# Kernel tuning notes

Hardware: AMD Instinct MI355X
Metric: run time of the kernel (lower is better)

## Reference

```python
import jax, jax.numpy as jnp
import numpy as np

T, B = 80, 256                 # timesteps (max objs per image), num sequences (images)
OBJ_DIM, EMBED, HID = 4096, 200, 512
NCLS = 151                      # 150 VG classes + background
D = HID + OBJ_DIM + EMBED + 128 # decoder inputs_dim = 4936


def _packed_gather_idx():
    # descending lengths 80..41, mimicking a sorted PackedSequence
    lengths = np.array([T - (i * 40) // B for i in range(B)])
    idx = []
    for t in range(T):
        bs = int((lengths > t).sum())
        idx.extend(t * B + b for b in range(bs))
    return np.asarray(idx, dtype=np.int32)  # [15504]


def setup_inputs() -> dict:
    key = jax.random.key(0)
    ks = jax.random.split(key, 6)
    s = jnp.float32(0.02)
    return {
        "sequence": jax.random.normal(ks[0], (T, B, D), jnp.float32),
        "embed": jax.random.normal(ks[1], (NCLS + 1, EMBED), jnp.float32) * s,
        "W_in": jax.random.normal(ks[2], (6 * HID, D + EMBED), jnp.float32) * s,
        "b_in": jnp.zeros((6 * HID,), jnp.float32),
        "W_state": jax.random.normal(ks[3], (5 * HID, HID), jnp.float32) * s,
        "b_state": jnp.zeros((5 * HID,), jnp.float32),
        "W_out": jax.random.normal(ks[4], (NCLS, HID), jnp.float32) * s,
        "b_out": jnp.zeros((NCLS,), jnp.float32),
        "gather_idx": jnp.asarray(_packed_gather_idx()),
    }


def reference(sequence, embed, W_in, b_in, W_state, b_state, W_out, b_out, gather_idx):
    H = HID

    def step(carry, x_t):
        h, c, prev_embed = carry
        ti = jnp.concatenate([x_t, prev_embed], axis=1)          # [B, D+E]
        pi = ti @ W_in.T + b_in                                   # [B, 6H]
        ps = h @ W_state.T + b_state                              # [B, 5H]
        i_g = jax.nn.sigmoid(pi[:, 0*H:1*H] + ps[:, 0*H:1*H])
        f_g = jax.nn.sigmoid(pi[:, 1*H:2*H] + ps[:, 1*H:2*H])
        m_i = jnp.tanh(pi[:, 2*H:3*H] + ps[:, 2*H:3*H])
        o_g = jax.nn.sigmoid(pi[:, 3*H:4*H] + ps[:, 3*H:4*H])
        c_new = i_g * m_i + f_g * c
        out = o_g * jnp.tanh(c_new)
        hw_g = jax.nn.sigmoid(pi[:, 4*H:5*H] + ps[:, 4*H:5*H])
        h_new = hw_g * out + (1.0 - hw_g) * pi[:, 5*H:6*H]        # highway
        pred = h_new @ W_out.T + b_out                            # [B, NCLS]
        # softmax is monotonic: argmax of softmax(pred)[:,1:] == argmax of pred[:,1:]
        best = jnp.argmax(pred[:, 1:], axis=1) + 1                # [B], in [1, NCLS-1]
        pe_new = embed[best + 1]                                  # [B, E]
        return (h_new, c_new, pe_new), (pred, best)

    h0 = jnp.zeros((B, HID), sequence.dtype)
    c0 = jnp.zeros((B, HID), sequence.dtype)
    pe0 = jnp.broadcast_to(embed[0], (B, EMBED))                  # 'start' token embed
    _, (dists, commits) = jax.lax.scan(step, (h0, c0, pe0), sequence)
    # packed (timestep-major) flattening of valid entries only
    out_dists = dists.reshape(T * B, NCLS)[gather_idx]            # [N, NCLS]
    out_commits = commits.reshape(T * B)[gather_idx]              # [N]
    return out_dists, out_commits
```

## Files before the change

### kernel.cpp

```cpp
#include <hip/hip_runtime.h>
#include <cstddef>
#include <cstdint>

#define T_STEPS 80
#define BATCH   256
#define DIM     4936
#define EMB     200
#define DE      5136
#define HID     512
#define SIXH    3072
#define FIVEH   2560
#define NCLS    151
#define NPACK   15504
#define NKT     156
#define NKT_H   16
#define NCOMB   2816

typedef unsigned short ushort_t;
typedef short short8 __attribute__((ext_vector_type(8)));
typedef float f32x4 __attribute__((ext_vector_type(4)));

__device__ inline ushort_t f2bf_rn(float x) {
    union { float f; uint32_t u; } v; v.f = x;
    uint32_t u = v.u;
    return (ushort_t)((u + 0x7FFFu + ((u >> 16) & 1u)) >> 16);
}
__device__ inline float bf2f(ushort_t b) {
    union { float f; uint32_t u; } v; v.u = ((uint32_t)b) << 16;
    return v.f;
}
__device__ inline float sigmoidf(float x) { return 1.f / (1.f + expf(-x)); }

__global__ __launch_bounds__(256) void convert_split(
    const float* __restrict__ src, int ld, int kvalid,
    ushort_t* __restrict__ hi, ushort_t* __restrict__ lo, int nktiles)
{
    __shared__ float s[128][33];
    const int tid = threadIdx.x;
    const int kt  = blockIdx.x;
    const int mt  = blockIdx.y;

#pragma unroll
    for (int it = 0; it < 4; ++it) {
        int idx = it * 256 + tid;
        int row = idx >> 3;
        int f4  = idx & 7;
        int k   = kt * 32 + f4 * 4;
        const float* p = src + (size_t)(mt * 128 + row) * ld + k;
        float4 v;
        if (k + 3 < kvalid) v = *(const float4*)p;
        else {
            v.x = (k + 0) < kvalid ? p[0] : 0.f;
            v.y = (k + 1) < kvalid ? p[1] : 0.f;
            v.z = (k + 2) < kvalid ? p[2] : 0.f;
            v.w = (k + 3) < kvalid ? p[3] : 0.f;
        }
        s[row][f4 * 4 + 0] = v.x; s[row][f4 * 4 + 1] = v.y;
        s[row][f4 * 4 + 2] = v.z; s[row][f4 * 4 + 3] = v.w;
    }
    __syncthreads();

    const size_t base = ((size_t)mt * nktiles + kt) * 4096;
#pragma unroll
    for (int it = 0; it < 2; ++it) {
        int o   = it * 256 + tid;
        int kb  = o >> 7;
        int row = o & 127;
        alignas(16) ushort_t hbuf[8];
        alignas(16) ushort_t lbuf[8];
#pragma unroll
        for (int e = 0; e < 8; ++e) {
            float x = s[row][kb * 8 + e];
            ushort_t hh = f2bf_rn(x);
            float lof = x - bf2f(hh);
            hbuf[e] = hh;
            lbuf[e] = f2bf_rn(lof);
        }
        *(uint4*)(hi + base + (size_t)o * 8) = *(const uint4*)hbuf;
        *(uint4*)(lo + base + (size_t)o * 8) = *(const uint4*)lbuf;
    }
}

__device__ inline void gload16(const ushort_t* g, ushort_t* l) {
    __builtin_amdgcn_global_load_lds(
        (const __attribute__((address_space(1))) void*)g,
        (__attribute__((address_space(3))) void*)l, 16, 0, 0);
}

__global__ __launch_bounds__(256) void mfma3(
    const ushort_t* __restrict__ Ah, const ushort_t* __restrict__ Al,
    const ushort_t* __restrict__ Bh, const ushort_t* __restrict__ Bl,
    const float* __restrict__ bias, float* __restrict__ OUT,
    int nkt, int ldout)
{
    __shared__ ushort_t sAh[2][4096], sAl[2][4096], sBh[2][4096], sBl[2][4096];

    const int tid  = threadIdx.x;
    const int wave = tid >> 6;
    const int lane = tid & 63;
    const int mt = blockIdx.y, ntb = blockIdx.x;
    const int wr = wave >> 1, wc = wave & 1;

    f32x4 acc[4][4];
#pragma unroll
    for (int i = 0; i < 4; ++i)
#pragma unroll
        for (int j = 0; j < 4; ++j) acc[i][j] = (f32x4){0.f, 0.f, 0.f, 0.f};

    const size_t abase = (size_t)mt * nkt * 4096;
    const size_t bbase = (size_t)ntb * nkt * 4096;
    const int lw = wave * 512;
    const int kb = lane >> 4;
    const int lr = lane & 15;
    const int aoff = kb * 1024 + (wr * 64 + lr) * 8;
    const int boff = kb * 1024 + (wc * 64 + lr) * 8;

#define STAGE_PX(buf, kt_) do {                                     \
        const size_t ko = (size_t)(kt_) * 4096 + tid * 8;           \
        gload16(Ah + abase + ko,        &sAh[buf][lw]);             \
        gload16(Ah + abase + ko + 2048, &sAh[buf][2048 + lw]);      \
        gload16(Al + abase + ko,        &sAl[buf][lw]);             \
        gload16(Al + abase + ko + 2048, &sAl[buf][2048 + lw]);      \
        gload16(Bh + bbase + ko,        &sBh[buf][lw]);             \
        gload16(Bh + bbase + ko + 2048, &sBh[buf][2048 + lw]);      \
        gload16(Bl + bbase + ko,        &sBl[buf][lw]);             \
        gload16(Bl + bbase + ko + 2048, &sBl[buf][2048 + lw]);      \
    } while (0)

    STAGE_PX(0, 0);
    asm volatile("s_waitcnt vmcnt(0)" ::: "memory");
    __builtin_amdgcn_s_barrier();

    int cur = 0;
    for (int kt = 0; kt < nkt; ++kt) {
        if (kt + 1 < nkt) STAGE_PX(cur ^ 1, kt + 1);

        const ushort_t* pAh = sAh[cur];
        const ushort_t* pAl = sAl[cur];
        const ushort_t* pBh = sBh[cur];
        const ushort_t* pBl = sBl[cur];
        short8 ah[4], al[4], bh[4], bl[4];
#pragma unroll
        for (int i = 0; i < 4; ++i) {
            ah[i] = *(const short8*)&pAh[aoff + i * 128];
            al[i] = *(const short8*)&pAl[aoff + i * 128];
        }
#pragma unroll
        for (int j = 0; j < 4; ++j) {
            bh[j] = *(const short8*)&pBh[boff + j * 128];
            bl[j] = *(const short8*)&pBl[boff + j * 128];
        }
#pragma unroll
        for (int i = 0; i < 4; ++i)
#pragma unroll
            for (int j = 0; j < 4; ++j) {
                acc[i][j] = __builtin_amdgcn_mfma_f32_16x16x32_bf16(ah[i], bh[j], acc[i][j], 0, 0, 0);
                acc[i][j] = __builtin_amdgcn_mfma_f32_16x16x32_bf16(ah[i], bl[j], acc[i][j], 0, 0, 0);
                acc[i][j] = __builtin_amdgcn_mfma_f32_16x16x32_bf16(al[i], bh[j], acc[i][j], 0, 0, 0);
            }

        __builtin_amdgcn_sched_barrier(0);
        asm volatile("s_waitcnt vmcnt(0)" ::: "memory");
        __builtin_amdgcn_s_barrier();
        cur ^= 1;
    }
#undef STAGE_PX

#pragma unroll
    for (int i = 0; i < 4; ++i) {
        const int row = mt * 128 + wr * 64 + i * 16 + (lane >> 4) * 4;
#pragma unroll
        for (int j = 0; j < 4; ++j) {
            const int col = ntb * 128 + wc * 64 + j * 16 + (lane & 15);
            const float bv = bias[col];
#pragma unroll
            for (int r = 0; r < 4; ++r)
                OUT[(size_t)(row + r) * ldout + col] = acc[i][j][r] + bv;
        }
    }
}

__global__ __launch_bounds__(256) void ps_splitk(
    const ushort_t* __restrict__ hH, const ushort_t* __restrict__ hL,
    const ushort_t* __restrict__ WcH, const ushort_t* __restrict__ WcL,
    float* __restrict__ partial)
{
    __shared__ ushort_t sAh[8192], sAl[8192], sBh[8192], sBl[8192];

    const int tid  = threadIdx.x;
    const int wave = tid >> 6;
    const int lane = tid & 63;
    const int ntile = blockIdx.x;
    const int mtile = blockIdx.y;
    const int ks    = blockIdx.z;
    const int amt = mtile >> 1, arh = mtile & 1;
    const int bmt = ntile >> 1, brh = ntile & 1;
    const int wr = wave >> 1, wc = wave & 1;

    f32x4 acc[2][2];
#pragma unroll
    for (int i = 0; i < 2; ++i)
#pragma unroll
        for (int j = 0; j < 2; ++j) acc[i][j] = (f32x4){0.f, 0.f, 0.f, 0.f};

    const int lw    = wave * 512;
    const int lsrcA = wave * 1024 + arh * 512 + lane * 8;
    const int lsrcB = wave * 1024 + brh * 512 + lane * 8;

#pragma unroll
    for (int ki = 0; ki < 4; ++ki) {
        const int kt = ks * 4 + ki;
        const size_t atile = ((size_t)(amt * NKT_H + kt)) * 4096;
        const size_t btile = ((size_t)(bmt * NKT_H + kt)) * 4096;
        gload16(hH  + atile + lsrcA, &sAh[ki * 2048 + lw]);
        gload16(hL  + atile + lsrcA, &sAl[ki * 2048 + lw]);
        gload16(WcH + btile + lsrcB, &sBh[ki * 2048 + lw]);
        gload16(WcL + btile + lsrcB, &sBl[ki * 2048 + lw]);
    }
    __syncthreads();

    const int kb = lane >> 4;
    const int lr = lane & 15;
#pragma unroll
    for (int ki = 0; ki < 4; ++ki) {
        short8 ah[2], al[2], bh[2], bl[2];
#pragma unroll
        for (int i = 0; i < 2; ++i) {
            const int ao = ki * 2048 + kb * 512 + (wr * 32 + i * 16 + lr) * 8;
            ah[i] = *(const short8*)&sAh[ao];
            al[i] = *(const short8*)&sAl[ao];
        }
#pragma unroll
        for (int j = 0; j < 2; ++j) {
            const int bo = ki * 2048 + kb * 512 + (wc * 32 + j * 16 + lr) * 8;
            bh[j] = *(const short8*)&sBh[bo];
            bl[j] = *(const short8*)&sBl[bo];
        }
#pragma unroll
        for (int i = 0; i < 2; ++i)
#pragma unroll
            for (int j = 0; j < 2; ++j) {
                acc[i][j] = __builtin_amdgcn_mfma_f32_16x16x32_bf16(ah[i], bh[j], acc[i][j], 0, 0, 0);
                acc[i][j] = __builtin_amdgcn_mfma_f32_16x16x32_bf16(ah[i], bl[j], acc[i][j], 0, 0, 0);
                acc[i][j] = __builtin_amdgcn_mfma_f32_16x16x32_bf16(al[i], bh[j], acc[i][j], 0, 0, 0);
            }
    }

    float* out = partial + ((size_t)ks * 256 + mtile * 64) * NCOMB + ntile * 64;
#pragma unroll
    for (int i = 0; i < 2; ++i) {
        const int row = wr * 32 + i * 16 + (lane >> 4) * 4;
#pragma unroll
        for (int j = 0; j < 2; ++j) {
            const int col = wc * 32 + j * 16 + (lane & 15);
#pragma unroll
            for (int r = 0; r < 4; ++r)
                out[(size_t)(row + r) * NCOMB + col] = acc[i][j][r];
        }
    }
}

__global__ __launch_bounds__(256) void ew_gemm(
    const float* __restrict__ embed, const float* __restrict__ Win,
    float* __restrict__ EW)
{
    __shared__ float As[16][68];
    __shared__ float Bs[16][68];
    const int tid = threadIdx.x;
    const int tx  = tid & 15;
    const int ty  = tid >> 4;
    const int n0  = blockIdx.x * 64;
    const int m0  = blockIdx.y * 64;
    const int lrow = tid >> 2;
    const int lk   = (tid & 3) * 4;

    float acc[4][4];
#pragma unroll
    for (int i = 0; i < 4; ++i)
#pragma unroll
        for (int j = 0; j < 4; ++j) acc[i][j] = 0.f;

    for (int k0 = 0; k0 < EMB; k0 += 16) {
        int k = k0 + lk;
        float4 av = {0.f,0.f,0.f,0.f}, bv = {0.f,0.f,0.f,0.f};
        if (k < EMB) {
            int am = m0 + lrow;
            if (am < 152) av = *(const float4*)(embed + (size_t)am * EMB + k);
            bv = *(const float4*)(Win + (size_t)(n0 + lrow) * DE + DIM + k);
        }
        __syncthreads();
        As[lk + 0][lrow] = av.x; As[lk + 1][lrow] = av.y;
        As[lk + 2][lrow] = av.z; As[lk + 3][lrow] = av.w;
        Bs[lk + 0][lrow] = bv.x; Bs[lk + 1][lrow] = bv.y;
        Bs[lk + 2][lrow] = bv.z; Bs[lk + 3][lrow] = bv.w;
        __syncthreads();
#pragma unroll
        for (int kk = 0; kk < 16; ++kk) {
            float4 a4 = *(const float4*)&As[kk][ty * 4];
            float4 b4 = *(const float4*)&Bs[kk][tx * 4];
            float avr[4] = {a4.x, a4.y, a4.z, a4.w};
            float bvr[4] = {b4.x, b4.y, b4.z, b4.w};
#pragma unroll
            for (int i = 0; i < 4; ++i)
#pragma unroll
                for (int j = 0; j < 4; ++j)
                    acc[i][j] = fmaf(avr[i], bvr[j], acc[i][j]);
        }
    }
#pragma unroll
    for (int i = 0; i < 4; ++i) {
        int m = m0 + ty * 4 + i;
        if (m < 152) {
#pragma unroll
            for (int j = 0; j < 4; ++j)
                EW[(size_t)m * SIXH + n0 + tx * 4 + j] = acc[i][j];
        }
    }
}

__global__ __launch_bounds__(256) void pad_wout(
    const float* __restrict__ Wout, float* __restrict__ padW)
{
    int i = blockIdx.x * 256 + threadIdx.x;
    if (i < 256 * 512) {
        int row = i >> 9;
        padW[i] = (row < NCLS) ? Wout[i] : 0.f;
    }
}

__global__ __launch_bounds__(256) void init_state(
    float* __restrict__ c, ushort_t* __restrict__ hHt, ushort_t* __restrict__ hLt)
{
    int i = blockIdx.x * 256 + threadIdx.x;
    if (i < BATCH * HID) { c[i] = 0.f; hHt[i] = 0; hLt[i] = 0; }
}

__global__ __launch_bounds__(256) void step_fused(
    const float* __restrict__ px_t,
    const float* __restrict__ EW,
    const float* __restrict__ partial,
    const float* __restrict__ b_state,
    const float* __restrict__ b_out,
    int first,
    ushort_t* __restrict__ hHt, ushort_t* __restrict__ hLt,
    float* __restrict__ c, float* __restrict__ hF,
    float* __restrict__ dists_prev,
    int*   __restrict__ commit_prev)
{
    __shared__ float hs[HID];
    __shared__ float preds_s[NCLS + 1];
    __shared__ int   commit_sh;

    const int tid = threadIdx.x;
    const int b   = blockIdx.x;

    int erow = 0;
    if (!first) {
        if (tid < NCLS) {
            const float* pq = partial + (size_t)b * NCOMB + 2560;
            float pr = b_out[tid] + pq[tid]
                     + pq[(size_t)256 * NCOMB + tid]
                     + pq[(size_t)2 * 256 * NCOMB + tid]
                     + pq[(size_t)3 * 256 * NCOMB + tid];
            preds_s[tid] = pr;
            dists_prev[(size_t)b * NCLS + tid] = pr;
        }
        __syncthreads();
        if (tid == 0) {
            int bi = 1; float bv = preds_s[1];
            for (int n = 2; n < NCLS; ++n) {
                float v = preds_s[n];
                if (v > bv) { bv = v; bi = n; }
            }
            commit_prev[b] = bi;
            commit_sh = bi;
        }
        __syncthreads();
        erow = commit_sh + 1;
    }

    const float* ew = EW + (size_t)erow * SIXH;
    const float* px = px_t + (size_t)b * SIXH;
    const float* pp = partial + (size_t)b * NCOMB;

#pragma unroll
    for (int it = 0; it < 2; ++it) {
        const int u = it * 256 + tid;
        float p[6];
#pragma unroll
        for (int k2 = 0; k2 < 5; ++k2) {
            const int o = k2 * HID + u;
            float s = pp[o] + pp[(size_t)256 * NCOMB + o]
                    + pp[(size_t)2 * 256 * NCOMB + o] + pp[(size_t)3 * 256 * NCOMB + o];
            p[k2] = px[o] + ew[o] + s + b_state[o];
        }
        p[5] = px[5 * HID + u] + ew[5 * HID + u];

        float i_g = sigmoidf(p[0]);
        float f_g = sigmoidf(p[1]);
        float m_i = tanhf(p[2]);
        float o_g = sigmoidf(p[3]);
        float c_new = i_g * m_i + f_g * c[(size_t)b * HID + u];
        float outv  = o_g * tanhf(c_new);
        float hw    = sigmoidf(p[4]);
        float h_new = hw * outv + (1.f - hw) * p[5];
        c[(size_t)b * HID + u]  = c_new;
        hF[(size_t)b * HID + u] = h_new;
        hs[u] = h_new;
    }
    __syncthreads();

    if (tid < 128) {
        const int half = tid >> 6;
        const int ch   = tid & 63;
        const int mt   = b >> 7;
        const int row  = b & 127;
        const size_t off = ((size_t)(mt * NKT_H + (ch >> 2))) * 4096
                         + (size_t)(ch & 3) * 1024 + (size_t)row * 8;
        alignas(16) ushort_t buf[8];
        if (half == 0) {
#pragma unroll
            for (int e = 0; e < 8; ++e) buf[e] = f2bf_rn(hs[ch * 8 + e]);
            *(uint4*)(hHt + off) = *(const uint4*)buf;
        } else {
#pragma unroll
            for (int e = 0; e < 8; ++e) {
                float x = hs[ch * 8 + e];
                buf[e] = f2bf_rn(x - bf2f(f2bf_rn(x)));
            }
            *(uint4*)(hLt + off) = *(const uint4*)buf;
        }
    }
}

__global__ __launch_bounds__(192) void finalize_last(
    const float* __restrict__ hF, const float* __restrict__ Wout,
    const float* __restrict__ b_out,
    float* __restrict__ dists_last, int* __restrict__ commits_last)
{
    __shared__ float hsh[HID];
    __shared__ float preds[NCLS + 1];
    const int b = blockIdx.x;
    const int tid = threadIdx.x;

    if (tid < 128) {
        float4 v = *(const float4*)(hF + (size_t)b * HID + tid * 4);
        *(float4*)&hsh[tid * 4] = v;
    }
    __syncthreads();
    if (tid < NCLS) {
        const float* w = Wout + (size_t)tid * HID;
        float s0 = 0.f, s1 = 0.f, s2 = 0.f, s3 = 0.f;
        for (int k = 0; k < HID; k += 4) {
            float4 w4 = *(const float4*)(w + k);
            float4 h4 = *(const float4*)&hsh[k];
            s0 = fmaf(h4.x, w4.x, s0);
            s1 = fmaf(h4.y, w4.y, s1);
            s2 = fmaf(h4.z, w4.z, s2);
            s3 = fmaf(h4.w, w4.w, s3);
        }
        float s = b_out[tid] + ((s0 + s1) + (s2 + s3));
        preds[tid] = s;
        dists_last[(size_t)b * NCLS + tid] = s;
    }
    __syncthreads();
    if (tid == 0) {
        int bi = 1; float bv = preds[1];
        for (int n = 2; n < NCLS; ++n) {
            float v = preds[n];
            if (v > bv) { bv = v; bi = n; }
        }
        commits_last[b] = bi;
    }
}

__global__ __launch_bounds__(192) void gather_out(
    const float* __restrict__ dists, const int* __restrict__ commits,
    const int* __restrict__ gidx, float* __restrict__ out)
{
    const int i = blockIdx.x;
    const int g = gidx[i];
    if (threadIdx.x < NCLS)
        out[(size_t)i * NCLS + threadIdx.x] = dists[(size_t)g * NCLS + threadIdx.x];
    if (threadIdx.x == NCLS)
        out[(size_t)NPACK * NCLS + i] = (float)commits[g];
}

extern "C" void kernel_launch(void* const* d_in, const int* in_sizes, int n_in,
                              void* d_out, int out_size, void* d_ws, size_t ws_size,
                              hipStream_t stream)
{
    const float* X      = (const float*)d_in[0];
    const float* embed  = (const float*)d_in[1];
    const float* Win    = (const float*)d_in[2];
    const float* b_in   = (const float*)d_in[3];
    const float* Wst    = (const float*)d_in[4];
    const float* b_st   = (const float*)d_in[5];
    const float* Wout   = (const float*)d_in[6];
    const float* b_out  = (const float*)d_in[7];
    const int*   gidx   = (const int*)d_in[8];

    const size_t WN  = (size_t)24 * NKT * 4096;
    const size_t WCN = (size_t)22 * NKT_H * 4096;
    const size_t HN  = (size_t)2 * NKT_H * 4096;

    ushort_t* Wh  = (ushort_t*)d_ws;
    ushort_t* Wl  = Wh + WN;
    ushort_t* WcH = Wl + WN;
    ushort_t* WcL = WcH + WCN;
    ushort_t* hHt = WcL + WCN;
    ushort_t* hLt = hHt + HN;
    float* EW      = (float*)(hLt + HN);
    float* partial = EW + (size_t)152 * SIXH;
    float* c       = partial + (size_t)4 * BATCH * NCOMB;
    float* hF      = c + (size_t)BATCH * HID;
    float* padW    = hF + (size_t)BATCH * HID;
    float* dists   = padW + (size_t)256 * HID;
    int* commits   = (int*)(dists + (size_t)T_STEPS * BATCH * NCLS);
    char* cbase    = (char*)(commits + T_STEPS * BATCH);

    size_t off = (size_t)(cbase - (char*)d_ws);
    off = (off + 255) & ~(size_t)255;
    const size_t per_t = (size_t)2 * 2 * NKT * 4096 * 2 + (size_t)BATCH * SIXH * 4;
    size_t rem = (ws_size > off) ? (ws_size - off) : 0;
    int CT = (int)(rem / per_t);
    if (CT > T_STEPS) CT = T_STEPS;
    if (CT < 1) CT = 1;

    ushort_t* Xh = (ushort_t*)((char*)d_ws + off);
    ushort_t* Xl = Xh + (size_t)2 * CT * NKT * 4096;
    float* px    = (float*)(Xl + (size_t)2 * CT * NKT * 4096);

    convert_split<<<dim3(NKT, 24), 256, 0, stream>>>(Win, DE, DIM, Wh, Wl, NKT);
    convert_split<<<dim3(NKT_H, 20), 256, 0, stream>>>(Wst, HID, HID, WcH, WcL, NKT_H);
    pad_wout<<<512, 256, 0, stream>>>(Wout, padW);
    convert_split<<<dim3(NKT_H, 2), 256, 0, stream>>>(
        padW, HID, HID, WcH + (size_t)20 * NKT_H * 4096, WcL + (size_t)20 * NKT_H * 4096, NKT_H);
    ew_gemm<<<dim3(SIXH / 64, 3), 256, 0, stream>>>(embed, Win, EW);
    init_state<<<512, 256, 0, stream>>>(c, hHt, hLt);

    for (int t0 = 0; t0 < T_STEPS; t0 += CT) {
        int nt = T_STEPS - t0;
        if (nt > CT) nt = CT;
        convert_split<<<dim3(NKT, 2 * nt), 256, 0, stream>>>(
            X + (size_t)t0 * BATCH * DIM, DIM, DIM, Xh, Xl, NKT);
        mfma3<<<dim3(SIXH / 128, 2 * nt), 256, 0, stream>>>(
            Xh, Xl, Wh, Wl, b_in, px, NKT, SIXH);
        for (int t = t0; t < t0 + nt; ++t) {
            const int tp = (t > 0) ? t - 1 : 0;
            ps_splitk<<<dim3(44, 4, 4), 256, 0, stream>>>(
                hHt, hLt, WcH, WcL, partial);
            step_fused<<<BATCH, 256, 0, stream>>>(
                px + (size_t)(t - t0) * BATCH * SIXH, EW, partial, b_st, b_out,
                (t == 0) ? 1 : 0, hHt, hLt, c, hF,
                dists + (size_t)tp * BATCH * NCLS, commits + (size_t)tp * BATCH);
        }
    }

    finalize_last<<<BATCH, 192, 0, stream>>>(
        hF, Wout, b_out,
        dists + (size_t)(T_STEPS - 1) * BATCH * NCLS,
        commits + (size_t)(T_STEPS - 1) * BATCH);

    gather_out<<<NPACK, 192, 0, stream>>>(dists, commits, gidx, (float*)d_out);
}
```

Before: 3.496 ms.

## Enlarge input-projection GEMM tile to 256 rows with triple-buffered LDS pipeline

The input-projection MFMA GEMM now uses 512-thread blocks that each compute a 256x128 tile instead of 128x128. This halves the number of blocks and lets each staged B (weight) tile be reused across twice as many rows, reducing global/L2 traffic. The double buffer is replaced with a three-slot dynamic-LDS ring (144 KB) that keeps two tiles in flight and waits with a partial vmcnt, so loads overlap with compute. The cost is one block per CU at launch_bounds(512,1) with heavy LDS use, which lowers occupancy and leaves less room for latency hiding through other blocks.

```diff
diff --git a/kernel.cpp b/kernel.cpp
--- a/kernel.cpp
+++ b/kernel.cpp
@@ -15,6 +15,7 @@
 #define NKT     156
 #define NKT_H   16
 #define NCOMB   2816
+#define BUFSZ   24576
 
 typedef unsigned short ushort_t;
 typedef short short8 __attribute__((ext_vector_type(8)));
@@ -87,18 +88,18 @@
         (__attribute__((address_space(3))) void*)l, 16, 0, 0);
 }
 
-__global__ __launch_bounds__(256) void mfma3(
+__global__ __launch_bounds__(512, 1) void mfma3(
     const ushort_t* __restrict__ Ah, const ushort_t* __restrict__ Al,
     const ushort_t* __restrict__ Bh, const ushort_t* __restrict__ Bl,
     const float* __restrict__ bias, float* __restrict__ OUT,
     int nkt, int ldout)
 {
-    __shared__ ushort_t sAh[2][4096], sAl[2][4096], sBh[2][4096], sBl[2][4096];
+    extern __shared__ __align__(16) ushort_t smem[];
 
     const int tid  = threadIdx.x;
     const int wave = tid >> 6;
     const int lane = tid & 63;
-    const int mt = blockIdx.y, ntb = blockIdx.x;
+    const int ntb = blockIdx.x, mtb = blockIdx.y;
     const int wr = wave >> 1, wc = wave & 1;
 
     f32x4 acc[4][4];
@@ -107,48 +108,52 @@
 #pragma unroll
         for (int j = 0; j < 4; ++j) acc[i][j] = (f32x4){0.f, 0.f, 0.f, 0.f};
 
-    const size_t abase = (size_t)mt * nkt * 4096;
-    const size_t bbase = (size_t)ntb * nkt * 4096;
-    const int lw = wave * 512;
+    const size_t a0 = (size_t)(2 * mtb) * nkt * 4096;
+    const size_t a1 = a0 + (size_t)nkt * 4096;
+    const size_t bb = (size_t)ntb * nkt * 4096;
+
     const int kb = lane >> 4;
     const int lr = lane & 15;
-    const int aoff = kb * 1024 + (wr * 64 + lr) * 8;
-    const int boff = kb * 1024 + (wc * 64 + lr) * 8;
-
-#define STAGE_PX(buf, kt_) do {                                     \
+    const int aoffl = (wr >> 1) * 4096 + kb * 1024 + ((wr & 1) * 64 + lr) * 8;
+    const int boffl = kb * 1024 + (wc * 64 + lr) * 8;
+
+#define STAGE3(slot, kt_) do {                                      \
+        ushort_t* d = smem + (slot) * BUFSZ;                        \
         const size_t ko = (size_t)(kt_) * 4096 + tid * 8;           \
-        gload16(Ah + abase + ko,        &sAh[buf][lw]);             \
-        gload16(Ah + abase + ko + 2048, &sAh[buf][2048 + lw]);      \
-        gload16(Al + abase + ko,        &sAl[buf][lw]);             \
-        gload16(Al + abase + ko + 2048, &sAl[buf][2048 + lw]);      \
-        gload16(Bh + bbase + ko,        &sBh[buf][lw]);             \
-        gload16(Bh + bbase + ko + 2048, &sBh[buf][2048 + lw]);      \
-        gload16(Bl + bbase + ko,        &sBl[buf][lw]);             \
-        gload16(Bl + bbase + ko + 2048, &sBl[buf][2048 + lw]);      \
+        gload16(Ah + a0 + ko, d + tid * 8);                         \
+        gload16(Ah + a1 + ko, d + 4096 + tid * 8);                  \
+        gload16(Al + a0 + ko, d + 8192 + tid * 8);                  \
+        gload16(Al + a1 + ko, d + 12288 + tid * 8);                 \
+        gload16(Bh + bb + ko, d + 16384 + tid * 8);                 \
+        gload16(Bl + bb + ko, d + 20480 + tid * 8);                 \
     } while (0)
 
-    STAGE_PX(0, 0);
-    asm volatile("s_waitcnt vmcnt(0)" ::: "memory");
-    __builtin_amdgcn_s_barrier();
-
-    int cur = 0;
+    STAGE3(0, 0);
+    if (nkt > 1) STAGE3(1, 1);
+
+    int cb = 0;
     for (int kt = 0; kt < nkt; ++kt) {
-        if (kt + 1 < nkt) STAGE_PX(cur ^ 1, kt + 1);
-
-        const ushort_t* pAh = sAh[cur];
-        const ushort_t* pAl = sAl[cur];
-        const ushort_t* pBh = sBh[cur];
-        const ushort_t* pBl = sBl[cur];
+        if (kt < nkt - 1) asm volatile("s_waitcnt vmcnt(6)" ::: "memory");
+        else              asm volatile("s_waitcnt vmcnt(0)" ::: "memory");
+        __builtin_amdgcn_sched_barrier(0);
+        __builtin_amdgcn_s_barrier();
+        if (kt + 2 < nkt) {
+            int s2 = cb + 2; if (s2 >= 3) s2 -= 3;
+            STAGE3(s2, kt + 2);
+        }
+
+        const ushort_t* p  = smem + cb * BUFSZ;
+        const ushort_t* pB = p + 16384;
         short8 ah[4], al[4], bh[4], bl[4];
 #pragma unroll
         for (int i = 0; i < 4; ++i) {
-            ah[i] = *(const short8*)&pAh[aoff + i * 128];
-            al[i] = *(const short8*)&pAl[aoff + i * 128];
+            ah[i] = *(const short8*)&p[aoffl + i * 128];
+            al[i] = *(const short8*)&p[8192 + aoffl + i * 128];
         }
 #pragma unroll
         for (int j = 0; j < 4; ++j) {
-            bh[j] = *(const short8*)&pBh[boff + j * 128];
-            bl[j] = *(const short8*)&pBl[boff + j * 128];
+            bh[j] = *(const short8*)&pB[boffl + j * 128];
+            bl[j] = *(const short8*)&pB[4096 + boffl + j * 128];
         }
 #pragma unroll
         for (int i = 0; i < 4; ++i)
@@ -159,16 +164,13 @@
                 acc[i][j] = __builtin_amdgcn_mfma_f32_16x16x32_bf16(al[i], bh[j], acc[i][j], 0, 0, 0);
             }
 
-        __builtin_amdgcn_sched_barrier(0);
-        asm volatile("s_waitcnt vmcnt(0)" ::: "memory");
-        __builtin_amdgcn_s_barrier();
-        cur ^= 1;
-    }
-#undef STAGE_PX
+        cb = (cb == 2) ? 0 : cb + 1;
+    }
+#undef STAGE3
 
 #pragma unroll
     for (int i = 0; i < 4; ++i) {
-        const int row = mt * 128 + wr * 64 + i * 16 + (lane >> 4) * 4;
+        const int row = mtb * 256 + wr * 64 + i * 16 + (lane >> 4) * 4;
 #pragma unroll
         for (int j = 0; j < 4; ++j) {
             const int col = ntb * 128 + wc * 64 + j * 16 + (lane & 15);
@@ -499,6 +501,10 @@
     const float* Wout   = (const float*)d_in[6];
     const float* b_out  = (const float*)d_in[7];
     const int*   gidx   = (const int*)d_in[8];
+
+    hipFuncSetAttribute((const void*)mfma3,
+                        hipFuncAttributeMaxDynamicSharedMemorySize,
+                        3 * BUFSZ * 2);
 
     const size_t WN  = (size_t)24 * NKT * 4096;
     const size_t WCN = (size_t)22 * NKT_H * 4096;
@@ -544,7 +550,7 @@
         if (nt > CT) nt = CT;
         convert_split<<<dim3(NKT, 2 * nt), 256, 0, stream>>>(
             X + (size_t)t0 * BATCH * DIM, DIM, DIM, Xh, Xl, NKT);
-        mfma3<<<dim3(SIXH / 128, 2 * nt), 256, 0, stream>>>(
+        mfma3<<<dim3(SIXH / 128, nt), 512, 3 * BUFSZ * 2, stream>>>(
             Xh, Xl, Wh, Wl, b_in, px, NKT, SIXH);
         for (int t = t0; t < t0 + nt; ++t) {
             const int tp = (t > 0) ? t - 1 : 0;
```

Result: faster. 3.259 ms (-6.8%).

## Load MFMA operands directly from global into registers, drop LDS staging

Applied to the files above, without the earlier changes.

The input-projection GEMM kernel no longer stages tiles through LDS with global_load_lds and barriers. Each wave now loads its hi/lo bf16 fragments straight from global memory into registers, using a two-set register double buffer. Blocks grow to 512 threads covering 256 rows, so each block handles two M tiles and the grid's M dimension halves. This removes LDS traffic and block-wide barriers, but operands shared between waves are no longer reused through LDS, so global/L2 load volume per block rises, and the doubled fragment registers may limit occupancy.

```diff
diff --git a/kernel.cpp b/kernel.cpp
--- a/kernel.cpp
+++ b/kernel.cpp
@@ -87,18 +87,16 @@
         (__attribute__((address_space(3))) void*)l, 16, 0, 0);
 }
 
-__global__ __launch_bounds__(256) void mfma3(
+__global__ __launch_bounds__(512, 2) void mfma3(
     const ushort_t* __restrict__ Ah, const ushort_t* __restrict__ Al,
     const ushort_t* __restrict__ Bh, const ushort_t* __restrict__ Bl,
     const float* __restrict__ bias, float* __restrict__ OUT,
     int nkt, int ldout)
 {
-    __shared__ ushort_t sAh[2][4096], sAl[2][4096], sBh[2][4096], sBl[2][4096];
-
     const int tid  = threadIdx.x;
     const int wave = tid >> 6;
     const int lane = tid & 63;
-    const int mt = blockIdx.y, ntb = blockIdx.x;
+    const int ntb = blockIdx.x, mtb = blockIdx.y;
     const int wr = wave >> 1, wc = wave & 1;
 
     f32x4 acc[4][4];
@@ -107,68 +105,59 @@
 #pragma unroll
         for (int j = 0; j < 4; ++j) acc[i][j] = (f32x4){0.f, 0.f, 0.f, 0.f};
 
-    const size_t abase = (size_t)mt * nkt * 4096;
-    const size_t bbase = (size_t)ntb * nkt * 4096;
-    const int lw = wave * 512;
     const int kb = lane >> 4;
     const int lr = lane & 15;
-    const int aoff = kb * 1024 + (wr * 64 + lr) * 8;
+    const size_t abase = ((size_t)(2 * mtb + (wr >> 1))) * nkt * 4096;
+    const size_t bbase = (size_t)ntb * nkt * 4096;
+    const int aoff = kb * 1024 + ((wr & 1) * 64 + lr) * 8;
     const int boff = kb * 1024 + (wc * 64 + lr) * 8;
 
-#define STAGE_PX(buf, kt_) do {                                     \
-        const size_t ko = (size_t)(kt_) * 4096 + tid * 8;           \
-        gload16(Ah + abase + ko,        &sAh[buf][lw]);             \
-        gload16(Ah + abase + ko + 2048, &sAh[buf][2048 + lw]);      \
-        gload16(Al + abase + ko,        &sAl[buf][lw]);             \
-        gload16(Al + abase + ko + 2048, &sAl[buf][2048 + lw]);      \
-        gload16(Bh + bbase + ko,        &sBh[buf][lw]);             \
-        gload16(Bh + bbase + ko + 2048, &sBh[buf][2048 + lw]);      \
-        gload16(Bl + bbase + ko,        &sBl[buf][lw]);             \
-        gload16(Bl + bbase + ko + 2048, &sBl[buf][2048 + lw]);      \
+    const ushort_t* pa_h = Ah + abase + aoff;
+    const ushort_t* pa_l = Al + abase + aoff;
+    const ushort_t* pb_h = Bh + bbase + boff;
+    const ushort_t* pb_l = Bl + bbase + boff;
+
+#define LOADSET(ah_, al_, bh_, bl_, kt_) do {                          \
+        const size_t o_ = (size_t)(kt_) * 4096;                        \
+        _Pragma("unroll")                                              \
+        for (int i_ = 0; i_ < 4; ++i_) {                               \
+            ah_[i_] = *(const short8*)(pa_h + o_ + i_ * 128);          \
+            al_[i_] = *(const short8*)(pa_l + o_ + i_ * 128);          \
+        }                                                              \
+        _Pragma("unroll")                                              \
+        for (int j_ = 0; j_ < 4; ++j_) {                               \
+            bh_[j_] = *(const short8*)(pb_h + o_ + j_ * 128);          \
+            bl_[j_] = *(const short8*)(pb_l + o_ + j_ * 128);          \
+        }                                                              \
     } while (0)
 
-    STAGE_PX(0, 0);
-    asm volatile("s_waitcnt vmcnt(0)" ::: "memory");
-    __builtin_amdgcn_s_barrier();
-
-    int cur = 0;
-    for (int kt = 0; kt < nkt; ++kt) {
-        if (kt + 1 < nkt) STAGE_PX(cur ^ 1, kt + 1);
-
-        const ushort_t* pAh = sAh[cur];
-        const ushort_t* pAl = sAl[cur];
-        const ushort_t* pBh = sBh[cur];
-        const ushort_t* pBl = sBl[cur];
-        short8 ah[4], al[4], bh[4], bl[4];
-#pragma unroll
-        for (int i = 0; i < 4; ++i) {
-            ah[i] = *(const short8*)&pAh[aoff + i * 128];
-            al[i] = *(const short8*)&pAl[aoff + i * 128];
-        }
-#pragma unroll
-        for (int j = 0; j < 4; ++j) {
-            bh[j] = *(const short8*)&pBh[boff + j * 128];
-            bl[j] = *(const short8*)&pBl[boff + j * 128];
-        }
-#pragma unroll
-        for (int i = 0; i < 4; ++i)
-#pragma unroll
-            for (int j = 0; j < 4; ++j) {
-                acc[i][j] = __builtin_amdgcn_mfma_f32_16x16x32_bf16(ah[i], bh[j], acc[i][j], 0, 0, 0);
-                acc[i][j] = __builtin_amdgcn_mfma_f32_16x16x32_bf16(ah[i], bl[j], acc[i][j], 0, 0, 0);
-                acc[i][j] = __builtin_amdgcn_mfma_f32_16x16x32_bf16(al[i], bh[j], acc[i][j], 0, 0, 0);
-            }
-
-        __builtin_amdgcn_sched_barrier(0);
-        asm volatile("s_waitcnt vmcnt(0)" ::: "memory");
-        __builtin_amdgcn_s_barrier();
-        cur ^= 1;
-    }
-#undef STAGE_PX
+#define MFMASET(ah_, al_, bh_, bl_) do {                               \
+        _Pragma("unroll")                                              \
+        for (int i_ = 0; i_ < 4; ++i_)                                 \
+            _Pragma("unroll")                                          \
+            for (int j_ = 0; j_ < 4; ++j_) {                           \
+                acc[i_][j_] = __builtin_amdgcn_mfma_f32_16x16x32_bf16(ah_[i_], bh_[j_], acc[i_][j_], 0, 0, 0); \
+                acc[i_][j_] = __builtin_amdgcn_mfma_f32_16x16x32_bf16(ah_[i_], bl_[j_], acc[i_][j_], 0, 0, 0); \
+                acc[i_][j_] = __builtin_amdgcn_mfma_f32_16x16x32_bf16(al_[i_], bh_[j_], acc[i_][j_], 0, 0, 0); \
+            }                                                          \
+    } while (0)
+
+    short8 ah0[4], al0[4], bh0[4], bl0[4];
+    short8 ah1[4], al1[4], bh1[4], bl1[4];
+
+    LOADSET(ah0, al0, bh0, bl0, 0);
+    for (int kt = 0; kt < nkt; kt += 2) {
+        if (kt + 1 < nkt) LOADSET(ah1, al1, bh1, bl1, kt + 1);
+        MFMASET(ah0, al0, bh0, bl0);
+        if (kt + 2 < nkt) LOADSET(ah0, al0, bh0, bl0, kt + 2);
+        if (kt + 1 < nkt) MFMASET(ah1, al1, bh1, bl1);
+    }
+#undef LOADSET
+#undef MFMASET
 
 #pragma unroll
     for (int i = 0; i < 4; ++i) {
-        const int row = mt * 128 + wr * 64 + i * 16 + (lane >> 4) * 4;
+        const int row = mtb * 256 + wr * 64 + i * 16 + (lane >> 4) * 4;
 #pragma unroll
         for (int j = 0; j < 4; ++j) {
             const int col = ntb * 128 + wc * 64 + j * 16 + (lane & 15);
@@ -544,7 +533,7 @@
         if (nt > CT) nt = CT;
         convert_split<<<dim3(NKT, 2 * nt), 256, 0, stream>>>(
             X + (size_t)t0 * BATCH * DIM, DIM, DIM, Xh, Xl, NKT);
-        mfma3<<<dim3(SIXH / 128, 2 * nt), 256, 0, stream>>>(
+        mfma3<<<dim3(SIXH / 128, nt), 512, 0, stream>>>(
             Xh, Xl, Wh, Wl, b_in, px, NKT, SIXH);
         for (int t = t0; t < t0 + nt; ++t) {
             const int tp = (t > 0) ? t - 1 : 0;
```

Measured after the change: 3.545 ms. Within noise of the previous version (+1.4%).
